# Optimization experiments

Hardware: AMD Instinct MI355X
Metric: run time of the kernel (lower is better)

Reference implementation:

```python
import jax, jax.numpy as jnp
import numpy as np
from jax import lax

DN = ('NCHW', 'OIHW', 'NCHW')
EPS = 1e-5

def conv2d(x, w):
    return lax.conv_general_dilated(x, w, (1, 1), 'VALID', dimension_numbers=DN)

def bn(x, g, b, m, v):
    # eval-mode BatchNorm2d, params shape [C]
    scale = (g / jnp.sqrt(v + EPS))[None, :, None, None]
    shift = (b - m * g / jnp.sqrt(v + EPS))[None, :, None, None]
    return x * scale + shift

def xcorr_depthwise(search, kernel):
    # search [B,C,Hs,Ws], kernel [B,C,hk,wk] -> [B,C,Hs-hk+1,Ws-wk+1]
    B, C, Hs, Ws = search.shape
    hk, wk = kernel.shape[2], kernel.shape[3]
    s = search.reshape(1, B * C, Hs, Ws)
    k = kernel.reshape(B * C, 1, hk, wk)
    out = lax.conv_general_dilated(s, k, (1, 1), 'VALID',
                                   dimension_numbers=DN,
                                   feature_group_count=B * C)
    return out.reshape(B, C, Hs - hk + 1, Ws - wk + 1)

def _bn_params(key, c):
    k1, k2, k3, k4 = jax.random.split(key, 4)
    g = jax.random.uniform(k1, (c,), jnp.float32, 0.5, 1.5)
    b = jax.random.normal(k2, (c,), jnp.float32) * 0.1
    m = jax.random.normal(k3, (c,), jnp.float32) * 0.1
    v = jax.random.uniform(k4, (c,), jnp.float32, 0.5, 1.5)
    return g, b, m, v

def setup_inputs() -> dict:
    key = jax.random.key(0)
    ks = jax.random.split(key, 10)
    IN, H, OUT = 256, 256, 10
    kernel = jax.random.normal(ks[0], (128, IN, 7, 7), jnp.float32)
    search = jax.random.normal(ks[1], (128, IN, 31, 31), jnp.float32)
    w_ck = jax.random.normal(ks[2], (H, IN, 3, 3), jnp.float32) * 0.05
    g1, b1, m1, v1 = _bn_params(ks[3], H)
    w_cs = jax.random.normal(ks[4], (H, IN, 3, 3), jnp.float32) * 0.05
    g2, b2, m2, v2 = _bn_params(ks[5], H)
    w_h1 = jax.random.normal(ks[6], (H, H, 1, 1), jnp.float32) * 0.05
    g3, b3, m3, v3 = _bn_params(ks[7], H)
    w_h2 = jax.random.normal(ks[8], (OUT, H, 1, 1), jnp.float32) * 0.05
    b_h2 = jax.random.normal(ks[9], (OUT,), jnp.float32) * 0.05
    return dict(kernel=kernel, search=search, w_ck=w_ck, g1=g1, b1=b1, m1=m1, v1=v1,
                w_cs=w_cs, g2=g2, b2=b2, m2=m2, v2=v2,
                w_h1=w_h1, g3=g3, b3=b3, m3=m3, v3=v3, w_h2=w_h2, b_h2=b_h2)

def reference(kernel, search, w_ck, g1, b1, m1, v1, w_cs, g2, b2, m2, v2,
              w_h1, g3, b3, m3, v3, w_h2, b_h2):
    # conv_kernel / conv_search branches: Conv3x3 -> BN -> ReLU
    k = jax.nn.relu(bn(conv2d(kernel, w_ck), g1, b1, m1, v1))   # [B,256,5,5]
    s = jax.nn.relu(bn(conv2d(search, w_cs), g2, b2, m2, v2))   # [B,256,29,29]
    # depthwise cross-correlation (search_crop/search_pos are None -> kernel_t = kernel)
    feat = xcorr_depthwise(s, k)                                 # [B,256,25,25]
    # head: Conv1x1 -> BN -> ReLU -> Conv1x1(+bias)
    h = jax.nn.relu(bn(conv2d(feat, w_h1), g3, b3, m3, v3))
    out = conv2d(h, w_h2) + b_h2[None, :, None, None]            # [B,10,25,25]
    return out
```

## Files before the change

kernel.cpp:

```cpp
#include <hip/hip_runtime.h>
#include <hip/hip_bf16.h>

#define EPS 1e-5f

typedef __attribute__((ext_vector_type(8))) short bf16x8;
typedef __attribute__((ext_vector_type(4))) float f32x4;
typedef __attribute__((ext_vector_type(4))) unsigned short u16x4;
typedef __attribute__((ext_vector_type(8))) unsigned short u16x8;

#define WAITVM8 asm volatile("s_waitcnt vmcnt(8)" ::: "memory")
#define WAITVM4 asm volatile("s_waitcnt vmcnt(4)" ::: "memory")
#define WAITVM2 asm volatile("s_waitcnt vmcnt(2)" ::: "memory")
#define WAITVM0 asm volatile("s_waitcnt vmcnt(0)" ::: "memory")
#define BAR()   __builtin_amdgcn_s_barrier()

__device__ __forceinline__ void gld_lds16(const void* g, void* l) {
    __builtin_amdgcn_global_load_lds(
        (const __attribute__((address_space(1))) unsigned int*)g,
        (__attribute__((address_space(3))) unsigned int*)l, 16, 0, 0);
}

#define RD8(RA, RB, SEL) do {                                                  \
    const int _b = (SEL) * 8192;                                               \
    _Pragma("unroll") for (int _i = 0; _i < 4; ++_i)                           \
        RA[_i] = *reinterpret_cast<const bf16x8*>(&lA[_b + aoff + _i * 512]);  \
    _Pragma("unroll") for (int _j = 0; _j < 4; ++_j)                           \
        RB[_j] = *reinterpret_cast<const bf16x8*>(&lB[_b + boff + _j * 512]);  \
} while (0)

#define RD4(RA4, SEL) do {                                                     \
    const int _b = (SEL) * 8192;                                               \
    _Pragma("unroll") for (int _i = 0; _i < 4; ++_i)                           \
        RA4[_i] = *reinterpret_cast<const bf16x8*>(                            \
            &lA[_b + aoff + (_i + 4) * 512]);                                  \
} while (0)

#define MFQ(RA, RB, I0) do {                                                   \
    _Pragma("unroll") for (int _i = 0; _i < 4; ++_i)                           \
    _Pragma("unroll") for (int _j = 0; _j < 4; ++_j)                           \
        acc[(I0) + _i][_j] = __builtin_amdgcn_mfma_f32_16x16x32_bf16(          \
            RA[_i], RB[_j], acc[(I0) + _i][_j], 0, 0, 0);                      \
} while (0)

#define STEP(CA0, CA4, CB, NA0, NB, SELT, STAGE_STMT, WAIT_STMT, DORD) do {    \
    RD4(CA4, (SELT));                                                          \
    STAGE_STMT;                                                                \
    __builtin_amdgcn_s_setprio(1); MFQ(CA0, CB, 0);                            \
    __builtin_amdgcn_s_setprio(0);                                             \
    WAIT_STMT;                                                                 \
    BAR();                                                                     \
    if (DORD) RD8(NA0, NB, ((SELT) + 1) & 3);                                  \
    __builtin_amdgcn_s_setprio(1); MFQ(CA4, CB, 4);                            \
    __builtin_amdgcn_s_setprio(0);                                             \
} while (0)

template<int HIN, int WIN, int NTOT>
__device__ __forceinline__ void conv_dev(
    int bid, int tid,
    __hip_bfloat16* lA, __hip_bfloat16* lB,
    const __hip_bfloat16* __restrict__ xt,
    const __hip_bfloat16* __restrict__ wt,
    const float* __restrict__ g, const float* __restrict__ bb,
    const float* __restrict__ mm_, const float* __restrict__ vv,
    __hip_bfloat16* __restrict__ y)
{
    constexpr int HOUT = HIN - 2, WOUT = WIN - 2, POUT = HOUT * WOUT;
    const int n0  = bid * 256;
    const int wid = tid >> 6, lane = tid & 63;
    const int wr = wid >> 2, wc = wid & 3;

    const int arow = tid >> 2;
    const int seg  = (tid & 3) ^ ((tid >> 3) & 3);

    const size_t wbase0 = (size_t)arow * 2304 + seg * 8;
    const size_t wbase1 = (size_t)(arow + 128) * 2304 + seg * 8;

    int nr0 = n0 + arow;       if (nr0 > NTOT - 1) nr0 = NTOT - 1;
    int nr1 = n0 + arow + 128; if (nr1 > NTOT - 1) nr1 = NTOT - 1;
    int b0 = nr0 / POUT, p0 = nr0 % POUT, oy0 = p0 / WOUT, ox0 = p0 % WOUT;
    int b1 = nr1 / POUT, p1 = nr1 % POUT, oy1 = p1 / WOUT, ox1 = p1 % WOUT;
    const size_t xbase0 = (((size_t)b0 * HIN + oy0) * WIN + ox0) * 256 + seg * 8;
    const size_t xbase1 = (((size_t)b1 * HIN + oy1) * WIN + ox1) * 256 + seg * 8;

    auto stage = [&](int c0, int j, int sel) {
        char* a0 = (char*)lA + sel * 16384 + wid * 1024;
        char* b0p = (char*)lB + sel * 16384 + wid * 1024;
        const int woff = j * 256 + c0;
        gld_lds16(wt + wbase0 + woff, a0);
        gld_lds16(wt + wbase1 + woff, a0 + 8192);
        const int xoff = ((j / 3) * WIN + (j % 3)) * 256 + c0;
        gld_lds16(xt + xbase0 + xoff, b0p);
        gld_lds16(xt + xbase1 + xoff, b0p + 8192);
    };

    f32x4 acc[8][4];
#pragma unroll
    for (int i = 0; i < 8; ++i)
#pragma unroll
        for (int j = 0; j < 4; ++j)
            acc[i][j] = f32x4{0.f, 0.f, 0.f, 0.f};

    const int l15 = lane & 15, l16 = lane >> 4;
    const int slot = l16 ^ ((l15 >> 1) & 3);
    const int aoff = (wr * 128 + l15) * 32 + slot * 8;
    const int boff = (wc * 64  + l15) * 32 + slot * 8;

    bf16x8 pA0[4], pA4[4], pB[4], qA0[4], qA4[4], qB[4];

    stage(0, 0, 0); stage(0, 1, 1); stage(0, 2, 2);
    int js = 3, c0s = 0;
    WAITVM8; BAR();
    RD8(pA0, pB, 0);

#define ADVC do { ++js; if (js == 9) { js = 0; c0s += 32; } } while (0)
    for (int tt = 0; tt < 17; ++tt) {
        STEP(pA0, pA4, pB, qA0, qB, 0, stage(c0s, js, 3), WAITVM8, true); ADVC;
        STEP(qA0, qA4, qB, pA0, pB, 1, stage(c0s, js, 0), WAITVM8, true); ADVC;
        STEP(pA0, pA4, pB, qA0, qB, 2, stage(c0s, js, 1), WAITVM8, true); ADVC;
        STEP(qA0, qA4, qB, pA0, pB, 3, stage(c0s, js, 2), WAITVM8, true); ADVC;
    }
    STEP(pA0, pA4, pB, qA0, qB, 0, stage(c0s, js, 3), WAITVM8, true);
    STEP(qA0, qA4, qB, pA0, pB, 1, (void)0,           WAITVM4, true);
    STEP(pA0, pA4, pB, qA0, qB, 2, (void)0,           WAITVM0, true);
    STEP(qA0, qA4, qB, pA0, pB, 3, (void)0,           (void)0, false);
#undef ADVC

#pragma unroll
    for (int i = 0; i < 8; ++i) {
        const int co_b = wr * 128 + i * 16 + l16 * 4;
        float sc[4], sh[4];
#pragma unroll
        for (int r = 0; r < 4; ++r) {
            sc[r] = g[co_b + r] * rsqrtf(vv[co_b + r] + EPS);
            sh[r] = bb[co_b + r] - mm_[co_b + r] * sc[r];
        }
#pragma unroll
        for (int jj = 0; jj < 4; ++jj) {
            const int n = n0 + wc * 64 + jj * 16 + l15;
            if (n < NTOT) {
                u16x4 o;
#pragma unroll
                for (int r = 0; r < 4; ++r) {
                    const float v = fmaxf(fmaf(acc[i][jj][r], sc[r], sh[r]), 0.f);
                    __hip_bfloat16 hv = __float2bfloat16(v);
                    o[r] = *reinterpret_cast<unsigned short*>(&hv);
                }
                *reinterpret_cast<u16x4*>(&y[(size_t)n * 256 + co_b]) = o;
            }
        }
    }
}

__global__ __launch_bounds__(512, 2) void conv_both(
    const __hip_bfloat16* __restrict__ xt_s, const __hip_bfloat16* __restrict__ wt_cs,
    const float* __restrict__ g2, const float* __restrict__ b2,
    const float* __restrict__ m2, const float* __restrict__ v2,
    __hip_bfloat16* __restrict__ y2,
    const __hip_bfloat16* __restrict__ xt_k, const __hip_bfloat16* __restrict__ wt_ck,
    const float* __restrict__ g1, const float* __restrict__ b1,
    const float* __restrict__ m1, const float* __restrict__ v1,
    __hip_bfloat16* __restrict__ y1)
{
    __shared__ __align__(16) __hip_bfloat16 lA[4 * 8192];
    __shared__ __align__(16) __hip_bfloat16 lB[4 * 8192];
    if (blockIdx.x < 421)
        conv_dev<31, 31, 107648>(blockIdx.x, threadIdx.x, lA, lB,
                                 xt_s, wt_cs, g2, b2, m2, v2, y2);
    else
        conv_dev<7, 7, 3200>(blockIdx.x - 421, threadIdx.x, lA, lB,
                             xt_k, wt_ck, g1, b1, m1, v1, y1);
}

__device__ __forceinline__ void nhwc_body(
    const float* __restrict__ x, __hip_bfloat16* __restrict__ xt, int P,
    int bx, int b, float* t )
{
    const int p0 = bx * 32;
    const float* xb = x + (size_t)b * 256 * P;
    const int pl = threadIdx.x & 31, cg = threadIdx.x >> 5;
#pragma unroll
    for (int it = 0; it < 32; ++it) {
        int c = cg + it * 8, p = p0 + pl;
        t[c * 33 + pl] = (p < P) ? xb[(size_t)c * P + p] : 0.f;
    }
    __syncthreads();
    const int p = threadIdx.x >> 3, l8 = threadIdx.x & 7;
    if (p0 + p < P) {
        __hip_bfloat16* xo = xt + ((size_t)b * P + p0 + p) * 256;
#pragma unroll
        for (int j = 0; j < 4; ++j) {
            const int c0 = j * 64 + l8 * 8;
            u16x8 o;
#pragma unroll
            for (int r = 0; r < 8; ++r) {
                __hip_bfloat16 hv = __float2bfloat16(t[(c0 + r) * 33 + p]);
                o[r] = *reinterpret_cast<unsigned short*>(&hv);
            }
            *reinterpret_cast<u16x8*>(&xo[c0]) = o;
        }
    }
}

__global__ __launch_bounds__(256) void prepass(
    const float* __restrict__ w_ck, __hip_bfloat16* __restrict__ wt_ck,
    const float* __restrict__ w_cs, __hip_bfloat16* __restrict__ wt_cs,
    const float* __restrict__ w_h1, __hip_bfloat16* __restrict__ wh1,
    const float* __restrict__ kernel, __hip_bfloat16* __restrict__ xt_k,
    const float* __restrict__ search, __hip_bfloat16* __restrict__ xt_s)
{
    __shared__ float t[256 * 33];
    const int bid = blockIdx.x;
    if (bid < 512) {
        const float* w = (bid < 256) ? w_ck : w_cs;
        __hip_bfloat16* wt = (bid < 256) ? wt_ck : wt_cs;
        const int co = bid & 255, ci = threadIdx.x;
        const float* wp = w + (size_t)co * 2304 + (size_t)ci * 9;
        __hip_bfloat16* wo = wt + (size_t)co * 2304 + ci;
#pragma unroll
        for (int j = 0; j < 9; ++j)
            wo[(size_t)j * 256] = __float2bfloat16(wp[j]);
    } else if (bid < 768) {
        const int i = (bid - 512) * 256 + threadIdx.x;
        wh1[i] = __float2bfloat16(w_h1[i]);
    } else if (bid < 1024) {
        const int idx = bid - 768;
        nhwc_body(kernel, xt_k, 49, idx & 1, idx >> 1, t);
    } else {
        const int idx = bid - 1024;
        nhwc_body(search, xt_s, 961, idx % 31, idx / 31, t);
    }
}

__global__ __launch_bounds__(512) void xcorr_head(
    const __hip_bfloat16* __restrict__ s,
    const __hip_bfloat16* __restrict__ k,
    const __hip_bfloat16* __restrict__ w1,
    const float* __restrict__ g, const float* __restrict__ bb,
    const float* __restrict__ mm_, const float* __restrict__ vv,
    const float* __restrict__ w2,
    const float* __restrict__ b2v,
    float* __restrict__ out)
{
    const int st = blockIdx.x, b = blockIdx.y;
    const int py0 = st * 5;
    const int tid = threadIdx.x;

    __shared__ __align__(16) __hip_bfloat16 featL[128 * 264];
    __shared__ __align__(16) __hip_bfloat16 lA[3 * 8192];

    {
        const int c = tid & 255, h = tid >> 8;
        const __hip_bfloat16* sp = s + (size_t)b * 841 * 256 + c;
        const __hip_bfloat16* kp = k + (size_t)b * 25 * 256 + c;
        float kv[25];
#pragma unroll
        for (int i = 0; i < 25; ++i)
            kv[i] = __bfloat162float(kp[(size_t)i * 256]);

        if (h == 0) {
            float acc3[3][25];
#pragma unroll
            for (int p = 0; p < 3; ++p)
#pragma unroll
                for (int px = 0; px < 25; ++px) acc3[p][px] = 0.f;
#pragma unroll
            for (int r = 0; r < 7; ++r) {
                float srow[29];
                const __hip_bfloat16* srp = sp + (size_t)(py0 + r) * 29 * 256;
#pragma unroll
                for (int rx = 0; rx < 29; ++rx)
                    srow[rx] = __bfloat162float(srp[(size_t)rx * 256]);
#pragma unroll
                for (int p = 0; p < 3; ++p) {
                    if (r >= p && r - p <= 4) {
                        const int ky = r - p;
#pragma unroll
                        for (int kx = 0; kx < 5; ++kx) {
                            const float kvv = kv[ky * 5 + kx];
#pragma unroll
                            for (int px = 0; px < 25; ++px)
                                acc3[p][px] = fmaf(srow[px + kx], kvv, acc3[p][px]);
                        }
                    }
                }
            }
#pragma unroll
            for (int p = 0; p < 3; ++p)
#pragma unroll
                for (int px = 0; px < 25; ++px)
                    featL[(p * 25 + px) * 264 + c] = __float2bfloat16(acc3[p][px]);
        } else {
            float acc2[2][25];
#pragma unroll
            for (int p = 0; p < 2; ++p)
#pragma unroll
                for (int px = 0; px < 25; ++px) acc2[p][px] = 0.f;
#pragma unroll
            for (int r = 3; r < 9; ++r) {
                float srow[29];
                const __hip_bfloat16* srp = sp + (size_t)(py0 + r) * 29 * 256;
#pragma unroll
                for (int rx = 0; rx < 29; ++rx)
                    srow[rx] = __bfloat162float(srp[(size_t)rx * 256]);
#pragma unroll
                for (int p = 3; p < 5; ++p) {
                    if (r >= p && r - p <= 4) {
                        const int ky = r - p;
#pragma unroll
                        for (int kx = 0; kx < 5; ++kx) {
                            const float kvv = kv[ky * 5 + kx];
#pragma unroll
                            for (int px = 0; px < 25; ++px)
                                acc2[p - 3][px] = fmaf(srow[px + kx], kvv, acc2[p - 3][px]);
                        }
                    }
                }
            }
#pragma unroll
            for (int p = 0; p < 2; ++p)
#pragma unroll
                for (int px = 0; px < 25; ++px)
                    featL[((p + 3) * 25 + px) * 264 + c] = __float2bfloat16(acc2[p][px]);
        }
    }
    __syncthreads();

    const int wid = tid >> 6, lane = tid & 63;
    const int wr = wid >> 2, wc = wid & 3;
    const int l15 = lane & 15, l16 = lane >> 4;
    const int seg  = (lane & 3) ^ ((lane >> 3) & 3);
    const int slot = l16 ^ ((l15 >> 1) & 3);
    const int aoff = (wr * 128 + l15) * 32 + slot * 8;

    auto stageA = [&](int c0, int sel) {
        char* dst = (char*)lA + sel * 16384 + wid * 2048;
        const size_t r0 = (size_t)(wid * 32 + (lane >> 2)) * 256;
        gld_lds16(w1 + r0 + c0 + seg * 8, dst);
        gld_lds16(w1 + r0 + 16 * 256 + c0 + seg * 8, dst + 1024);
    };

    f32x4 acc[8][2];
#pragma unroll
    for (int i = 0; i < 8; ++i) {
        acc[i][0] = f32x4{0.f, 0.f, 0.f, 0.f};
        acc[i][1] = f32x4{0.f, 0.f, 0.f, 0.f};
    }

#define RDH(AF, BF, SEL, C0) do {                                              \
    const int _b = (SEL) * 8192;                                               \
    _Pragma("unroll") for (int _i = 0; _i < 8; ++_i)                           \
        AF[_i] = *reinterpret_cast<const bf16x8*>(&lA[_b + aoff + _i * 512]);  \
    _Pragma("unroll") for (int _j = 0; _j < 2; ++_j)                           \
        BF[_j] = *reinterpret_cast<const bf16x8*>(                             \
            &featL[(wc * 32 + _j * 16 + l15) * 264 + (C0) + l16 * 8]);         \
} while (0)

#define MFH(AF, BF) do {                                                       \
    __builtin_amdgcn_s_setprio(1);                                             \
    _Pragma("unroll") for (int _i = 0; _i < 8; ++_i)                           \
    _Pragma("unroll") for (int _j = 0; _j < 2; ++_j)                           \
        acc[_i][_j] = __builtin_amdgcn_mfma_f32_16x16x32_bf16(                 \
            AF[_i], BF[_j], acc[_i][_j], 0, 0, 0);                             \
    __builtin_amdgcn_s_setprio(0);                                             \
} while (0)

    {
        bf16x8 af[8], bf[2];
        stageA(0, 0); stageA(32, 1);
        WAITVM2; BAR();
        RDH(af, bf, 0, 0);   stageA(64, 2);  MFH(af, bf);
        WAITVM2; BAR();
        RDH(af, bf, 1, 32);  stageA(96, 0);  MFH(af, bf);
        WAITVM2; BAR();
        RDH(af, bf, 2, 64);  stageA(128, 1); MFH(af, bf);
        WAITVM2; BAR();
        RDH(af, bf, 0, 96);  stageA(160, 2); MFH(af, bf);
        WAITVM2; BAR();
        RDH(af, bf, 1, 128); stageA(192, 0); MFH(af, bf);
        WAITVM2; BAR();
        RDH(af, bf, 2, 160); stageA(224, 1); MFH(af, bf);
        WAITVM2; BAR();
        RDH(af, bf, 0, 192);                 MFH(af, bf);
        WAITVM0; BAR();
        RDH(af, bf, 1, 224);                 MFH(af, bf);
    }
#undef RDH
#undef MFH

    __syncthreads();
    float* lw   = (float*)lA;
    float* lred = lw + 2816;
    for (int t = tid; t < 2560; t += 512) lw[t] = w2[t];
    if (tid < 10) lw[2560 + tid] = b2v[tid];
    __syncthreads();

    float p[2][10];
#pragma unroll
    for (int jj = 0; jj < 2; ++jj)
#pragma unroll
        for (int o = 0; o < 10; ++o) p[jj][o] = 0.f;

#pragma unroll
    for (int i = 0; i < 8; ++i) {
        const int co_b = wr * 128 + i * 16 + l16 * 4;
        float sc[4], sh[4];
#pragma unroll
        for (int r = 0; r < 4; ++r) {
            sc[r] = g[co_b + r] * rsqrtf(vv[co_b + r] + EPS);
            sh[r] = bb[co_b + r] - mm_[co_b + r] * sc[r];
        }
        float w4[10][4];
#pragma unroll
        for (int o = 0; o < 10; ++o) {
            f32x4 wv = *reinterpret_cast<const f32x4*>(&lw[o * 256 + co_b]);
#pragma unroll
            for (int r = 0; r < 4; ++r) w4[o][r] = wv[r];
        }
#pragma unroll
        for (int jj = 0; jj < 2; ++jj) {
            float hv[4];
#pragma unroll
            for (int r = 0; r < 4; ++r)
                hv[r] = fmaxf(fmaf(acc[i][jj][r], sc[r], sh[r]), 0.f);
#pragma unroll
            for (int o = 0; o < 10; ++o)
#pragma unroll
                for (int r = 0; r < 4; ++r)
                    p[jj][o] = fmaf(hv[r], w4[o][r], p[jj][o]);
        }
    }

#pragma unroll
    for (int jj = 0; jj < 2; ++jj)
#pragma unroll
        for (int o = 0; o < 10; ++o) {
            float v = p[jj][o];
            v += __shfl_xor(v, 16, 64);
            v += __shfl_xor(v, 32, 64);
            p[jj][o] = v;
        }

    if (wr == 0 && l16 == 0) {
#pragma unroll
        for (int jj = 0; jj < 2; ++jj)
#pragma unroll
            for (int o = 0; o < 10; ++o)
                lred[((wc * 2 + jj) * 16 + l15) * 10 + o] = p[jj][o];
    }
    __syncthreads();
    if (wr == 1) {
#pragma unroll
        for (int jj = 0; jj < 2; ++jj) {
            const int n = wc * 32 + jj * 16 + l15;
            if (n < 125) {
                const int py = py0 + n / 25, pxc = n % 25;
#pragma unroll
                for (int t = 0; t < 3; ++t) {
                    const int o = l16 + 4 * t;
                    if (o < 10) {
                        float v = p[jj][o]
                                + lred[((wc * 2 + jj) * 16 + l15) * 10 + o]
                                + lw[2560 + o];
                        out[(((size_t)b * 10 + o) * 25 + py) * 25 + pxc] = v;
                    }
                }
            }
        }
    }
}

extern "C" void kernel_launch(void* const* d_in, const int* in_sizes, int n_in,
                              void* d_out, int out_size, void* d_ws, size_t ws_size,
                              hipStream_t stream) {
    const float* kernel = (const float*)d_in[0];
    const float* search = (const float*)d_in[1];
    const float* w_ck   = (const float*)d_in[2];
    const float* g1 = (const float*)d_in[3];
    const float* b1 = (const float*)d_in[4];
    const float* m1 = (const float*)d_in[5];
    const float* v1 = (const float*)d_in[6];
    const float* w_cs   = (const float*)d_in[7];
    const float* g2 = (const float*)d_in[8];
    const float* b2 = (const float*)d_in[9];
    const float* m2 = (const float*)d_in[10];
    const float* v2 = (const float*)d_in[11];
    const float* w_h1   = (const float*)d_in[12];
    const float* g3 = (const float*)d_in[13];
    const float* b3 = (const float*)d_in[14];
    const float* m3 = (const float*)d_in[15];
    const float* v3 = (const float*)d_in[16];
    const float* w_h2   = (const float*)d_in[17];
    const float* b_h2   = (const float*)d_in[18];

    float* out = (float*)d_out;

    __hip_bfloat16* ws = (__hip_bfloat16*)d_ws;
    __hip_bfloat16* y1    = ws;
    __hip_bfloat16* y2    = ws + (size_t)819200;
    __hip_bfloat16* wt_ck = ws + (size_t)28377088;
    __hip_bfloat16* wt_cs = ws + (size_t)28966912;
    __hip_bfloat16* wh1   = ws + (size_t)29556736;
    __hip_bfloat16* xt_k  = ws + (size_t)29622272;
    __hip_bfloat16* xt_s  = ws + (size_t)31227904;

    (void)in_sizes; (void)n_in; (void)out_size; (void)ws_size;

    prepass<<<4992, 256, 0, stream>>>(w_ck, wt_ck, w_cs, wt_cs, w_h1, wh1,
                                      kernel, xt_k, search, xt_s);

    conv_both<<<434, 512, 0, stream>>>(xt_s, wt_cs, g2, b2, m2, v2, y2,
                                       xt_k, wt_ck, g1, b1, m1, v1, y1);

    xcorr_head<<<dim3(5, 128), 512, 0, stream>>>(
        y2, y1, wh1, g3, b3, m3, v3, w_h2, b_h2, out);
}
```

Before: 266.6 us.

## Switch conv GEMM to double-buffered K=64 tiles with simpler pipeline

Replaces the 4-stage K=32 LDS ring with fine-grained split LDS reads and MFMA interleaving by a 2-stage double buffer using K=64 tiles. Each stage now loads 8 global-to-LDS chunks per thread, with a new 8-way XOR swizzle. Each compute step reads all A and B fragments up front and then issues 64 MFMAs. This halves the number of barriers and iterations, but it waits for vmcnt(0) every step, so prefetch depth shrinks and register pressure from holding 24 fragments rises.

```diff
diff --git a/kernel.cpp b/kernel.cpp
--- a/kernel.cpp
+++ b/kernel.cpp
@@ -8,8 +8,6 @@
 typedef __attribute__((ext_vector_type(4))) unsigned short u16x4;
 typedef __attribute__((ext_vector_type(8))) unsigned short u16x8;
 
-#define WAITVM8 asm volatile("s_waitcnt vmcnt(8)" ::: "memory")
-#define WAITVM4 asm volatile("s_waitcnt vmcnt(4)" ::: "memory")
 #define WAITVM2 asm volatile("s_waitcnt vmcnt(2)" ::: "memory")
 #define WAITVM0 asm volatile("s_waitcnt vmcnt(0)" ::: "memory")
 #define BAR()   __builtin_amdgcn_s_barrier()
@@ -19,40 +17,6 @@
         (const __attribute__((address_space(1))) unsigned int*)g,
         (__attribute__((address_space(3))) unsigned int*)l, 16, 0, 0);
 }
-
-#define RD8(RA, RB, SEL) do {                                                  \
-    const int _b = (SEL) * 8192;                                               \
-    _Pragma("unroll") for (int _i = 0; _i < 4; ++_i)                           \
-        RA[_i] = *reinterpret_cast<const bf16x8*>(&lA[_b + aoff + _i * 512]);  \
-    _Pragma("unroll") for (int _j = 0; _j < 4; ++_j)                           \
-        RB[_j] = *reinterpret_cast<const bf16x8*>(&lB[_b + boff + _j * 512]);  \
-} while (0)
-
-#define RD4(RA4, SEL) do {                                                     \
-    const int _b = (SEL) * 8192;                                               \
-    _Pragma("unroll") for (int _i = 0; _i < 4; ++_i)                           \
-        RA4[_i] = *reinterpret_cast<const bf16x8*>(                            \
-            &lA[_b + aoff + (_i + 4) * 512]);                                  \
-} while (0)
-
-#define MFQ(RA, RB, I0) do {                                                   \
-    _Pragma("unroll") for (int _i = 0; _i < 4; ++_i)                           \
-    _Pragma("unroll") for (int _j = 0; _j < 4; ++_j)                           \
-        acc[(I0) + _i][_j] = __builtin_amdgcn_mfma_f32_16x16x32_bf16(          \
-            RA[_i], RB[_j], acc[(I0) + _i][_j], 0, 0, 0);                      \
-} while (0)
-
-#define STEP(CA0, CA4, CB, NA0, NB, SELT, STAGE_STMT, WAIT_STMT, DORD) do {    \
-    RD4(CA4, (SELT));                                                          \
-    STAGE_STMT;                                                                \
-    __builtin_amdgcn_s_setprio(1); MFQ(CA0, CB, 0);                            \
-    __builtin_amdgcn_s_setprio(0);                                             \
-    WAIT_STMT;                                                                 \
-    BAR();                                                                     \
-    if (DORD) RD8(NA0, NB, ((SELT) + 1) & 3);                                  \
-    __builtin_amdgcn_s_setprio(1); MFQ(CA4, CB, 4);                            \
-    __builtin_amdgcn_s_setprio(0);                                             \
-} while (0)
 
 template<int HIN, int WIN, int NTOT>
 __device__ __forceinline__ void conv_dev(
@@ -69,28 +33,31 @@
     const int wid = tid >> 6, lane = tid & 63;
     const int wr = wid >> 2, wc = wid & 3;
 
-    const int arow = tid >> 2;
-    const int seg  = (tid & 3) ^ ((tid >> 3) & 3);
-
-    const size_t wbase0 = (size_t)arow * 2304 + seg * 8;
-    const size_t wbase1 = (size_t)(arow + 128) * 2304 + seg * 8;
-
-    int nr0 = n0 + arow;       if (nr0 > NTOT - 1) nr0 = NTOT - 1;
-    int nr1 = n0 + arow + 128; if (nr1 > NTOT - 1) nr1 = NTOT - 1;
-    int b0 = nr0 / POUT, p0 = nr0 % POUT, oy0 = p0 / WOUT, ox0 = p0 % WOUT;
-    int b1 = nr1 / POUT, p1 = nr1 % POUT, oy1 = p1 / WOUT, ox1 = p1 % WOUT;
-    const size_t xbase0 = (((size_t)b0 * HIN + oy0) * WIN + ox0) * 256 + seg * 8;
-    const size_t xbase1 = (((size_t)b1 * HIN + oy1) * WIN + ox1) * 256 + seg * 8;
+    const int srow8 = wid * 8 + (lane >> 3);
+    const int sseg  = (lane & 7) ^ ((lane >> 3) & 7);
+
+    size_t wb[4], xb[4];
+#pragma unroll
+    for (int q = 0; q < 4; ++q) {
+        wb[q] = (size_t)(q * 64 + srow8) * 2304 + sseg * 8;
+        int nr = n0 + q * 64 + srow8; if (nr > NTOT - 1) nr = NTOT - 1;
+        int b_ = nr / POUT, p_ = nr % POUT, oy = p_ / WOUT, ox = p_ % WOUT;
+        xb[q] = (((size_t)b_ * HIN + oy) * WIN + ox) * 256 + sseg * 8;
+    }
 
     auto stage = [&](int c0, int j, int sel) {
-        char* a0 = (char*)lA + sel * 16384 + wid * 1024;
-        char* b0p = (char*)lB + sel * 16384 + wid * 1024;
+        char* aD = (char*)lA + sel * 32768 + wid * 1024;
+        char* bD = (char*)lB + sel * 32768 + wid * 1024;
         const int woff = j * 256 + c0;
-        gld_lds16(wt + wbase0 + woff, a0);
-        gld_lds16(wt + wbase1 + woff, a0 + 8192);
+        gld_lds16(wt + wb[0] + woff, aD);
+        gld_lds16(wt + wb[1] + woff, aD + 8192);
+        gld_lds16(wt + wb[2] + woff, aD + 16384);
+        gld_lds16(wt + wb[3] + woff, aD + 24576);
         const int xoff = ((j / 3) * WIN + (j % 3)) * 256 + c0;
-        gld_lds16(xt + xbase0 + xoff, b0p);
-        gld_lds16(xt + xbase1 + xoff, b0p + 8192);
+        gld_lds16(xt + xb[0] + xoff, bD);
+        gld_lds16(xt + xb[1] + xoff, bD + 8192);
+        gld_lds16(xt + xb[2] + xoff, bD + 16384);
+        gld_lds16(xt + xb[3] + xoff, bD + 24576);
     };
 
     f32x4 acc[8][4];
@@ -101,28 +68,54 @@
             acc[i][j] = f32x4{0.f, 0.f, 0.f, 0.f};
 
     const int l15 = lane & 15, l16 = lane >> 4;
-    const int slot = l16 ^ ((l15 >> 1) & 3);
-    const int aoff = (wr * 128 + l15) * 32 + slot * 8;
-    const int boff = (wc * 64  + l15) * 32 + slot * 8;
-
-    bf16x8 pA0[4], pA4[4], pB[4], qA0[4], qA4[4], qB[4];
-
-    stage(0, 0, 0); stage(0, 1, 1); stage(0, 2, 2);
-    int js = 3, c0s = 0;
-    WAITVM8; BAR();
-    RD8(pA0, pB, 0);
-
-#define ADVC do { ++js; if (js == 9) { js = 0; c0s += 32; } } while (0)
+    const int sL = l16 ^ (l15 & 7);
+    const int aoffL = (wr * 128 + l15) * 64 + sL * 8;
+    const int boffL = (wc * 64  + l15) * 64 + sL * 8;
+
+    auto cmp = [&](int sel) {
+        const int base = sel * 16384;
+        bf16x8 aL[8], aH[8], bL[4], bH[4];
+#pragma unroll
+        for (int i = 0; i < 8; ++i)
+            aL[i] = *reinterpret_cast<const bf16x8*>(&lA[base + aoffL + i * 1024]);
+#pragma unroll
+        for (int i = 0; i < 8; ++i)
+            aH[i] = *reinterpret_cast<const bf16x8*>(&lA[base + (aoffL ^ 32) + i * 1024]);
+#pragma unroll
+        for (int j = 0; j < 4; ++j)
+            bL[j] = *reinterpret_cast<const bf16x8*>(&lB[base + boffL + j * 1024]);
+#pragma unroll
+        for (int j = 0; j < 4; ++j)
+            bH[j] = *reinterpret_cast<const bf16x8*>(&lB[base + (boffL ^ 32) + j * 1024]);
+        __builtin_amdgcn_s_setprio(1);
+#pragma unroll
+        for (int i = 0; i < 8; ++i)
+#pragma unroll
+            for (int j = 0; j < 4; ++j)
+                acc[i][j] = __builtin_amdgcn_mfma_f32_16x16x32_bf16(
+                    aL[i], bL[j], acc[i][j], 0, 0, 0);
+        __builtin_amdgcn_s_setprio(0);
+        __builtin_amdgcn_s_setprio(1);
+#pragma unroll
+        for (int i = 0; i < 8; ++i)
+#pragma unroll
+            for (int j = 0; j < 4; ++j)
+                acc[i][j] = __builtin_amdgcn_mfma_f32_16x16x32_bf16(
+                    aH[i], bH[j], acc[i][j], 0, 0, 0);
+        __builtin_amdgcn_s_setprio(0);
+    };
+
+    stage(0, 0, 0);
+    int js = 1, c0s = 0;
+    WAITVM0; BAR();
+
+#define ADVC do { ++js; if (js == 9) { js = 0; c0s += 64; } } while (0)
     for (int tt = 0; tt < 17; ++tt) {
-        STEP(pA0, pA4, pB, qA0, qB, 0, stage(c0s, js, 3), WAITVM8, true); ADVC;
-        STEP(qA0, qA4, qB, pA0, pB, 1, stage(c0s, js, 0), WAITVM8, true); ADVC;
-        STEP(pA0, pA4, pB, qA0, qB, 2, stage(c0s, js, 1), WAITVM8, true); ADVC;
-        STEP(qA0, qA4, qB, pA0, pB, 3, stage(c0s, js, 2), WAITVM8, true); ADVC;
-    }
-    STEP(pA0, pA4, pB, qA0, qB, 0, stage(c0s, js, 3), WAITVM8, true);
-    STEP(qA0, qA4, qB, pA0, pB, 1, (void)0,           WAITVM4, true);
-    STEP(pA0, pA4, pB, qA0, qB, 2, (void)0,           WAITVM0, true);
-    STEP(qA0, qA4, qB, pA0, pB, 3, (void)0,           (void)0, false);
+        stage(c0s, js, 1); ADVC; cmp(0); WAITVM0; BAR();
+        stage(c0s, js, 0); ADVC; cmp(1); WAITVM0; BAR();
+    }
+    stage(c0s, js, 1); cmp(0); WAITVM0; BAR();
+    cmp(1);
 #undef ADVC
 
 #pragma unroll
@@ -161,8 +154,8 @@
     const float* __restrict__ m1, const float* __restrict__ v1,
     __hip_bfloat16* __restrict__ y1)
 {
-    __shared__ __align__(16) __hip_bfloat16 lA[4 * 8192];
-    __shared__ __align__(16) __hip_bfloat16 lB[4 * 8192];
+    __shared__ __align__(16) __hip_bfloat16 lA[2 * 16384];
+    __shared__ __align__(16) __hip_bfloat16 lB[2 * 16384];
     if (blockIdx.x < 421)
         conv_dev<31, 31, 107648>(blockIdx.x, threadIdx.x, lA, lB,
                                  xt_s, wt_cs, g2, b2, m2, v2, y2);
```

Measured after the change: 270.5 us. Within noise of the previous version (+1.5%).
